# Optimization experiments

Hardware: AMD Instinct MI355X
Metric: run time of the kernel (lower is better)

Reference implementation:

```python
import jax, jax.numpy as jnp
import numpy as np

B, L, E = 4, 1024, 1024
H = 16
HD = E // H
CLIP = 16
SCALE = 1.0 / np.sqrt(HD)


def setup_inputs() -> dict:
    key = jax.random.key(0)
    ks = jax.random.split(key, 13)
    def lin(k, fan_in, fan_out, gain):
        # xavier_uniform
        limit = gain * np.sqrt(6.0 / (fan_in + fan_out))
        return jax.random.uniform(k, (fan_out, fan_in), jnp.float32, -limit, limit)
    inv_sqrt2 = 1.0 / np.sqrt(2.0)
    return {
        "query": jax.random.normal(ks[0], (B, L, E), jnp.float32),
        "key": jax.random.normal(ks[1], (B, L, E), jnp.float32),
        "value": jax.random.normal(ks[2], (B, L, E), jnp.float32),
        "wq": lin(ks[3], E, E, inv_sqrt2), "bq": jnp.zeros((E,), jnp.float32),
        "wk": lin(ks[4], E, E, inv_sqrt2), "bk": jnp.zeros((E,), jnp.float32),
        "wv": lin(ks[5], E, E, inv_sqrt2), "bv": jnp.zeros((E,), jnp.float32),
        "wo": lin(ks[6], E, E, 1.0), "bo": jnp.zeros((E,), jnp.float32),
        "rel_k": jax.random.normal(ks[7], (2 * CLIP + 1, HD), jnp.float32) * 0.02,
        "rel_v": jax.random.normal(ks[8], (2 * CLIP + 1, HD), jnp.float32) * 0.02,
    }


def _heads(x):  # (B, L, E) -> (B, H, L, HD)
    return x.reshape(B, L, H, HD).transpose(0, 2, 1, 3)


def reference(query, key, value, wq, bq, wk, bk, wv, bv, wo, bo, rel_k, rel_v):
    q = _heads(query @ wq.T + bq)
    k = _heads(key @ wk.T + bk)
    v = _heads(value @ wv.T + bv)

    # relative-position index matrix (L_q, L_k), clipped to [-CLIP, CLIP]
    pos = jnp.arange(L)
    dist = jnp.clip(pos[None, :] - pos[:, None], -CLIP, CLIP) + CLIP
    r_k = rel_k[dist]  # (L, L, HD)
    r_v = rel_v[dist]  # (L, L, HD)

    dot = jnp.einsum('bhid,bhjd->bhij', q, k)
    rel = jnp.einsum('bhid,ijd->bhij', q, r_k)
    scores = (dot + rel) * SCALE
    attn = jax.nn.softmax(scores, axis=-1)

    y = jnp.einsum('bhij,bhjd->bhid', attn, v) + jnp.einsum('bhij,ijd->bhid', attn, r_v)
    y = y.transpose(0, 2, 1, 3).reshape(B, L, E)
    return y @ wo.T + bo
```

## Files before the change

kernel.cpp:

```cpp
#include <hip/hip_runtime.h>

#define BB 4
#define LL 1024
#define EE 1024
#define HH 16
#define HD 64
#define NBUCKET 33
#define SCALE 0.125f
#define SC2 (0.125f * 1.44269504088896f)

typedef unsigned short u16;
using f32x4 = __attribute__((ext_vector_type(4))) float;
using s16x8 = __attribute__((ext_vector_type(8))) short;

__device__ __forceinline__ u16 f2bf(float f) {
  union { float f; unsigned u; } x; x.f = f;
  unsigned r = (x.u + 0x7fffu + ((x.u >> 16) & 1u)) >> 16;
  return (u16)r;
}

__device__ __forceinline__ void gld_lds16(const void* g, void* s) {
  __builtin_amdgcn_global_load_lds((const __attribute__((address_space(1))) void*)g,
                                   (__attribute__((address_space(3))) void*)s, 16, 0, 0);
}

__device__ __forceinline__ float qsum16(float s) {
  s += __shfl_xor(s, 1); s += __shfl_xor(s, 2);
  s += __shfl_xor(s, 4); s += __shfl_xor(s, 8);
  return s;
}

__global__ __launch_bounds__(256) void cvt_all(
    const float* __restrict__ q, const float* __restrict__ k, const float* __restrict__ v,
    const float* __restrict__ wq, const float* __restrict__ wk, const float* __restrict__ wv,
    const float* __restrict__ wo, const float* __restrict__ rk,
    u16* __restrict__ oq, u16* __restrict__ ok, u16* __restrict__ ov,
    u16* __restrict__ owq, u16* __restrict__ owk, u16* __restrict__ owv,
    u16* __restrict__ owo, u16* __restrict__ ork) {
  const int bid = blockIdx.x;
  const int tid = threadIdx.x;
  if (bid < 12288) {
    const int z = bid >> 12;
    const int i = (bid & 4095) * 256 + tid;
    const float* in = z == 0 ? q : (z == 1 ? k : v);
    u16* out = z == 0 ? oq : (z == 1 ? ok : ov);
    float4 f = ((const float4*)in)[i];
    ushort4 o;
    o.x = f2bf(f.x); o.y = f2bf(f.y); o.z = f2bf(f.z); o.w = f2bf(f.w);
    ((ushort4*)out)[i] = o;
  } else if (bid < 16384) {
    const int z = (bid - 12288) >> 10;
    const int i = ((bid - 12288) & 1023) * 256 + tid;
    const float* in = z == 0 ? wq : (z == 1 ? wk : (z == 2 ? wv : wo));
    u16* out = z == 0 ? owq : (z == 1 ? owk : (z == 2 ? owv : owo));
    float4 f = ((const float4*)in)[i];
    ushort4 o;
    o.x = f2bf(f.x); o.y = f2bf(f.y); o.z = f2bf(f.z); o.w = f2bf(f.w);
    ((ushort4*)out)[i] = o;
  } else {
    const int i = (bid - 16384) * 256 + tid;
    ork[i] = (i < 33 * 64) ? f2bf(rk[i]) : (u16)0;
  }
}

template <int MODE>
__device__ __forceinline__ void gemm128_bt(const u16* __restrict__ A,
                                           const u16* __restrict__ Bw,
                                           const float* __restrict__ bias,
                                           u16* __restrict__ obf,
                                           float* __restrict__ ofp,
                                           int M, int N, int K, int m0, int n0) {
  __shared__ u16 a_sm[128 * 64];
  __shared__ u16 b_sm[128 * 64];
  const int tid = threadIdx.x;
  const int wave = tid >> 6, lane = tid & 63;
  const int row16 = lane & 15, quad = lane >> 4;
  const int wr = (wave >> 1) * 64, wc = (wave & 1) * 64;
  const int srow = lane >> 3, scol = (lane & 7) * 8;

  f32x4 acc[4][4] = {};

  for (int k0 = 0; k0 < K; k0 += 64) {
#pragma unroll
    for (int t = 0; t < 4; ++t) {
      const int chunk = wave * 4 + t;
      const int r = chunk * 8 + srow;
      gld_lds16(A + (size_t)(m0 + r) * K + k0 + scol, a_sm + chunk * 512);
      gld_lds16(Bw + (size_t)(n0 + r) * K + k0 + scol, b_sm + chunk * 512);
    }
    __syncthreads();
#pragma unroll
    for (int ks = 0; ks < 2; ++ks) {
      s16x8 af[4], bf[4];
#pragma unroll
      for (int mi = 0; mi < 4; ++mi)
        af[mi] = *(const s16x8*)&a_sm[(wr + mi * 16 + row16) * 64 + ks * 32 + quad * 8];
#pragma unroll
      for (int ni = 0; ni < 4; ++ni)
        bf[ni] = *(const s16x8*)&b_sm[(wc + ni * 16 + row16) * 64 + ks * 32 + quad * 8];
#pragma unroll
      for (int mi = 0; mi < 4; ++mi)
#pragma unroll
        for (int ni = 0; ni < 4; ++ni)
          acc[mi][ni] = __builtin_amdgcn_mfma_f32_16x16x32_bf16(af[mi], bf[ni], acc[mi][ni], 0, 0, 0);
    }
    __syncthreads();
  }

#pragma unroll
  for (int mi = 0; mi < 4; ++mi)
#pragma unroll
    for (int ni = 0; ni < 4; ++ni) {
      const int n = n0 + wc + ni * 16 + row16;
      const float bn = bias[n];
      if (MODE == 2) {
        const int mr0 = m0 + wr + mi * 16 + quad * 4;
        const int b = mr0 >> 10, l = mr0 & 1023;
        const int h = n >> 6, hd = n & 63;
        ushort4 o;
        o.x = f2bf(acc[mi][ni][0] + bn);
        o.y = f2bf(acc[mi][ni][1] + bn);
        o.z = f2bf(acc[mi][ni][2] + bn);
        o.w = f2bf(acc[mi][ni][3] + bn);
        *(ushort4*)&obf[((size_t)((b * HH + h) * HD + hd)) * LL + l] = o;
      } else {
#pragma unroll
        for (int r = 0; r < 4; ++r) {
          const int m = m0 + wr + mi * 16 + quad * 4 + r;
          const float v = acc[mi][ni][r] + bn;
          if (MODE == 0) {
            const int b = m >> 10, l = m & 1023, h = n >> 6, hd = n & 63;
            obf[((size_t)((b * HH + h) * LL + l)) * HD + hd] = f2bf(v);
          } else {
            ofp[(size_t)m * N + n] = v;
          }
        }
      }
    }
}

__global__ __launch_bounds__(256) void proj_gemm(
    const u16* __restrict__ xq, const u16* __restrict__ xk, const u16* __restrict__ xv,
    const u16* __restrict__ wqb, const u16* __restrict__ wkb, const u16* __restrict__ wvb,
    const float* __restrict__ bq, const float* __restrict__ bk, const float* __restrict__ bv,
    u16* __restrict__ oq, u16* __restrict__ ok, u16* __restrict__ ovt) {
  if (blockIdx.z == 0)
    gemm128_bt<0>(xq, wqb, bq, oq, nullptr, BB * LL, EE, EE, blockIdx.y * 128, blockIdx.x * 128);
  else if (blockIdx.z == 1)
    gemm128_bt<0>(xk, wkb, bk, ok, nullptr, BB * LL, EE, EE, blockIdx.y * 128, blockIdx.x * 128);
  else
    gemm128_bt<2>(xv, wvb, bv, ovt, nullptr, BB * LL, EE, EE, blockIdx.y * 128, blockIdx.x * 128);
}

__global__ __launch_bounds__(256) void out_gemm(const u16* __restrict__ Y,
                                                const u16* __restrict__ wob,
                                                const float* __restrict__ bo,
                                                float* __restrict__ out) {
  gemm128_bt<1>(Y, wob, bo, nullptr, out, BB * LL, EE, EE, blockIdx.y * 128, blockIdx.x * 128);
}

__global__ __launch_bounds__(256) void attn_fused(
    const u16* __restrict__ Q, const u16* __restrict__ Kb, const u16* __restrict__ Vt,
    const u16* __restrict__ RKp, const float* __restrict__ RV, u16* __restrict__ Y) {
  __shared__ __align__(16) float qr_sm[4][16 * 36];
  __shared__ __align__(16) float s_sm[4][16 * 36];
  __shared__ __align__(16) unsigned char kv[2][17408];

  const int tid = threadIdx.x;
  const int wave = tid >> 6, lane = tid & 63;
  const int row16 = lane & 15, quad = lane >> 4;
  const int bh = blockIdx.x & 63;
  const int i0 = (blockIdx.x >> 6) * 64;
  const int wq0 = i0 + wave * 16;
  const u16* qp = Q + (size_t)bh * LL * HD;
  const char* kpB = (const char*)(Kb + (size_t)bh * LL * HD);
  const char* vpB = (const char*)(Vt + (size_t)bh * HD * LL);

  float* qr_w = &qr_sm[wave][0];
  float* s_w = &s_sm[wave][0];

  int srcK[2], srcV[2];
#pragma unroll
  for (int t = 0; t < 2; ++t) {
    const int cK = (wave * 2 + t) * 64 + lane;
    const int rw = cK >> 3;
    const int cb = ((cK * 16) & 127) ^ ((rw & 7) << 4);
    srcK[t] = rw * 128 + cb;
    srcV[t] = rw * 2048 + cb;
  }
  const int swz = (row16 & 7) << 4;

#pragma unroll
  for (int t = 0; t < 2; ++t) {
    gld_lds16(kpB + srcK[t], kv[0] + (wave * 2 + t) * 1024);
    gld_lds16(vpB + srcV[t], kv[0] + 9216 + (wave * 2 + t) * 1024);
  }

  for (int t = lane; t < 16 * 36; t += 64) s_w[t] = 0.f;

  s16x8 qf[2];
#pragma unroll
  for (int ks = 0; ks < 2; ++ks)
    qf[ks] = *(const s16x8*)(qp + (size_t)(wq0 + row16) * HD + ks * 32 + quad * 8);

  f32x4 a0, a2;
#pragma unroll
  for (int nt = 0; nt < 3; ++nt) {
    f32x4 a = {};
#pragma unroll
    for (int ks = 0; ks < 2; ++ks) {
      s16x8 bfr = *(const s16x8*)(RKp + (size_t)(nt * 16 + row16) * HD + ks * 32 + quad * 8);
      a = __builtin_amdgcn_mfma_f32_16x16x32_bf16(qf[ks], bfr, a, 0, 0, 0);
    }
    if (nt == 0) a0 = a;
    if (nt == 2) a2 = a;
    const int idx = nt * 16 + row16;
    if (idx < NBUCKET)
#pragma unroll
      for (int r = 0; r < 4; ++r) qr_w[(quad * 4 + r) * 36 + idx] = a[r];
  }
  float blo[4], bhi[4];
#pragma unroll
  for (int r = 0; r < 4; ++r) {
    blo[r] = __shfl(a0[r], lane & 48);
    bhi[r] = __shfl(a2[r], lane & 48);
  }

  f32x4 oacc[4] = {};
  float rsum[4] = {0.f, 0.f, 0.f, 0.f};
  float plos[4] = {0.f, 0.f, 0.f, 0.f};
  float phis[4] = {0.f, 0.f, 0.f, 0.f};
  int dbase[4];
#pragma unroll
  for (int nt = 0; nt < 4; ++nt) dbase[nt] = nt * 16 + row16 - quad * 4 - wq0;

  asm volatile("s_waitcnt vmcnt(0) lgkmcnt(0)" ::: "memory");
  __builtin_amdgcn_s_barrier();
  __builtin_amdgcn_sched_barrier(0);

  for (int jt = 0; jt < 16; ++jt) {
    const int j0 = jt * 64;
    unsigned char* kcur = (unsigned char*)kv[jt & 1];
    unsigned char* knxt = (unsigned char*)kv[(jt & 1) ^ 1];
    u16* p_w = (u16*)(kcur) + wave * 1152;

    if (jt < 15) {
      const size_t j1 = (size_t)(j0 + 64);
#pragma unroll
      for (int t = 0; t < 2; ++t) {
        gld_lds16(kpB + j1 * 128 + srcK[t], knxt + (wave * 2 + t) * 1024);
        gld_lds16(vpB + j1 * 2 + srcV[t], knxt + 9216 + (wave * 2 + t) * 1024);
      }
    }

    f32x4 sacc[4] = {};
#pragma unroll
    for (int ks = 0; ks < 2; ++ks)
#pragma unroll
      for (int nt2 = 0; nt2 < 4; ++nt2) {
        const int L = (nt2 * 16 + row16) * 128 + ks * 64 + quad * 16;
        const s16x8 kfr = *(const s16x8*)(kcur + (L ^ swz));
        sacc[nt2] = __builtin_amdgcn_mfma_f32_16x16x32_bf16(qf[ks], kfr, sacc[nt2], 0, 0, 0);
      }
    asm volatile("s_waitcnt lgkmcnt(0)" ::: "memory");
    __builtin_amdgcn_s_barrier();
    __builtin_amdgcn_sched_barrier(0);

    float p[4][4];
    const bool far_lo = (wq0 >= j0 + 79);
    const bool far_hi = (j0 >= wq0 + 31);
    if (far_lo || far_hi) {
#pragma unroll
      for (int r = 0; r < 4; ++r) {
        const float bias = far_lo ? blo[r] : bhi[r];
        float acc = 0.f;
#pragma unroll
        for (int nt2 = 0; nt2 < 4; ++nt2) {
          const float pv = exp2f((sacc[nt2][r] + bias) * SC2);
          p[nt2][r] = pv;
          acc += pv;
        }
        rsum[r] += acc;
        if (far_lo) plos[r] += acc; else phis[r] += acc;
      }
    } else {
#pragma unroll
      for (int nt2 = 0; nt2 < 4; ++nt2)
#pragma unroll
        for (int r = 0; r < 4; ++r) {
          const int dr = dbase[nt2] + j0 - r;
          int bk = dr < -16 ? -16 : (dr > 16 ? 16 : dr);
          bk += 16;
          const float bias = qr_w[(quad * 4 + r) * 36 + bk];
          const float pv = exp2f((sacc[nt2][r] + bias) * SC2);
          p[nt2][r] = pv;
          rsum[r] += pv;
          if (dr <= -16) plos[r] += pv;
          else if (dr >= 16) phis[r] += pv;
          else atomicAdd(&s_w[(quad * 4 + r) * 36 + bk], pv);
        }
    }

#pragma unroll
    for (int nt2 = 0; nt2 < 4; ++nt2) {
      const int c = nt2 * 16 + row16;
#pragma unroll
      for (int rr = 0; rr < 2; ++rr) {
        unsigned pk;
        asm("v_cvt_pk_bf16_f32 %0, %1, %2" : "=v"(pk)
            : "v"(p[nt2][rr * 2]), "v"(p[nt2][rr * 2 + 1]));
        p_w[(quad * 4 + rr * 2) * 72 + c] = (u16)pk;
        p_w[(quad * 4 + rr * 2 + 1) * 72 + c] = (u16)(pk >> 16);
      }
    }

#pragma unroll
    for (int ks = 0; ks < 2; ++ks) {
      const s16x8 pf = *(const s16x8*)&p_w[row16 * 72 + ks * 32 + quad * 8];
#pragma unroll
      for (int dt = 0; dt < 4; ++dt) {
        const int L = (dt * 16 + row16) * 128 + ks * 64 + quad * 16;
        const s16x8 vfr = *(const s16x8*)(kcur + 9216 + (L ^ swz));
        oacc[dt] = __builtin_amdgcn_mfma_f32_16x16x32_bf16(pf, vfr, oacc[dt], 0, 0, 0);
      }
    }

    asm volatile("s_waitcnt vmcnt(0) lgkmcnt(0)" ::: "memory");
    __builtin_amdgcn_s_barrier();
    __builtin_amdgcn_sched_barrier(0);
  }

  float lacc[4], slo[4], shi[4];
#pragma unroll
  for (int r = 0; r < 4; ++r) {
    lacc[r] = qsum16(rsum[r]);
    slo[r] = qsum16(plos[r]);
    shi[r] = qsum16(phis[r]);
  }

  float* rv_sm = (float*)kv[0];
  for (int t = tid; t < NBUCKET * HD; t += 256) rv_sm[t] = RV[t];
  __syncthreads();

  const int b = bh >> 4, h = bh & 15;
#pragma unroll
  for (int r = 0; r < 4; ++r) {
    const int i_loc = quad * 4 + r;
    float rel[4] = {0.f, 0.f, 0.f, 0.f};
    for (int bk = 0; bk < NBUCKET; ++bk) {
      float sv = s_w[i_loc * 36 + bk];
      if (bk == 0) sv += slo[r];
      if (bk == 32) sv += shi[r];
#pragma unroll
      for (int dt = 0; dt < 4; ++dt) rel[dt] += sv * rv_sm[bk * HD + dt * 16 + row16];
    }
    const float inv = 1.0f / lacc[r];
#pragma unroll
    for (int dt = 0; dt < 4; ++dt) {
      const float y = (oacc[dt][r] + rel[dt]) * inv;
      Y[((size_t)(b * LL + wq0 + i_loc)) * EE + h * HD + dt * 16 + row16] = f2bf(y);
    }
  }
}

extern "C" void kernel_launch(void* const* d_in, const int* in_sizes, int n_in,
                              void* d_out, int out_size, void* d_ws, size_t ws_size,
                              hipStream_t stream) {
  const float* query = (const float*)d_in[0];
  const float* key_  = (const float*)d_in[1];
  const float* value = (const float*)d_in[2];
  const float* wq = (const float*)d_in[3];
  const float* bq = (const float*)d_in[4];
  const float* wk = (const float*)d_in[5];
  const float* bk = (const float*)d_in[6];
  const float* wv = (const float*)d_in[7];
  const float* bv = (const float*)d_in[8];
  const float* wo = (const float*)d_in[9];
  const float* bo = (const float*)d_in[10];
  const float* rel_k = (const float*)d_in[11];
  const float* rel_v = (const float*)d_in[12];

  char* base = (char*)d_ws;
  size_t off = 0;
  auto alloc = [&](size_t bytes) -> void* {
    void* p = base + off;
    off += (bytes + 255) & ~(size_t)255;
    return p;
  };
  const size_t XE = (size_t)BB * LL * EE;
  u16* xq    = (u16*)alloc(XE * 2);
  u16* xk    = (u16*)alloc(XE * 2);
  u16* xv    = (u16*)alloc(XE * 2);
  u16* wqb   = (u16*)alloc((size_t)EE * EE * 2);
  u16* wkb   = (u16*)alloc((size_t)EE * EE * 2);
  u16* wvb   = (u16*)alloc((size_t)EE * EE * 2);
  u16* wob   = (u16*)alloc((size_t)EE * EE * 2);
  u16* q_ws  = (u16*)alloc(XE * 2);
  u16* k_ws  = (u16*)alloc(XE * 2);
  u16* vt_ws = (u16*)alloc(XE * 2);
  u16* relkp = (u16*)alloc(48 * 64 * 2);
  u16* y_ws = xq;

  cvt_all<<<16396, 256, 0, stream>>>(query, key_, value, wq, wk, wv, wo, rel_k,
                                     xq, xk, xv, wqb, wkb, wvb, wob, relkp);

  proj_gemm<<<dim3(EE / 128, BB * LL / 128, 3), 256, 0, stream>>>(
      xq, xk, xv, wqb, wkb, wvb, bq, bk, bv, q_ws, k_ws, vt_ws);

  attn_fused<<<1024, 256, 0, stream>>>(q_ws, k_ws, vt_ws, relkp, rel_v, y_ws);

  out_gemm<<<dim3(EE / 128, BB * LL / 128), 256, 0, stream>>>(y_ws, wob, bo, (float*)d_out);
}
```

Baseline: 278.8 us.

## Transpose attention MFMAs to keep P in registers and drop LDS double buffering

Swaps the MFMA operand order so scores come out transposed (key rows per lane, query columns per lane). P can then be repacked in registers with permlane32 swaps instead of a round trip through LDS. A permuted K row mapping lines the score layout up with the PV operand, and the row-sum reductions become cross-quad shuffles. The K/V tile is now single-buffered, so each iteration waits on its own global loads before computing, which gives up the previous load/compute overlap in exchange for less LDS use and fewer LDS writes.

```diff
diff --git a/kernel.cpp b/kernel.cpp
--- a/kernel.cpp
+++ b/kernel.cpp
@@ -22,12 +22,6 @@
 __device__ __forceinline__ void gld_lds16(const void* g, void* s) {
   __builtin_amdgcn_global_load_lds((const __attribute__((address_space(1))) void*)g,
                                    (__attribute__((address_space(3))) void*)s, 16, 0, 0);
-}
-
-__device__ __forceinline__ float qsum16(float s) {
-  s += __shfl_xor(s, 1); s += __shfl_xor(s, 2);
-  s += __shfl_xor(s, 4); s += __shfl_xor(s, 8);
-  return s;
 }
 
 __global__ __launch_bounds__(256) void cvt_all(
@@ -162,9 +156,9 @@
 __global__ __launch_bounds__(256) void attn_fused(
     const u16* __restrict__ Q, const u16* __restrict__ Kb, const u16* __restrict__ Vt,
     const u16* __restrict__ RKp, const float* __restrict__ RV, u16* __restrict__ Y) {
-  __shared__ __align__(16) float qr_sm[4][16 * 36];
+  __shared__ __align__(16) float qr_sm[4][576];
   __shared__ __align__(16) float s_sm[4][16 * 36];
-  __shared__ __align__(16) unsigned char kv[2][17408];
+  __shared__ __align__(16) unsigned char kv[16384];
 
   const int tid = threadIdx.x;
   const int wave = tid >> 6, lane = tid & 63;
@@ -188,12 +182,16 @@
     srcK[t] = rw * 128 + cb;
     srcV[t] = rw * 2048 + cb;
   }
-  const int swz = (row16 & 7) << 4;
+  const int q2 = row16 >> 2;
+  const int prow = ((((q2 << 1) | (q2 >> 1)) & 3) << 2) + (row16 & 3);
+  const int swzK = (prow & 7) << 4;
+  const int swzV = (row16 & 7) << 4;
+  const int rho4 = (((quad << 1) | (quad >> 1)) & 3) << 2;
 
 #pragma unroll
   for (int t = 0; t < 2; ++t) {
-    gld_lds16(kpB + srcK[t], kv[0] + (wave * 2 + t) * 1024);
-    gld_lds16(vpB + srcV[t], kv[0] + 9216 + (wave * 2 + t) * 1024);
+    gld_lds16(kpB + srcK[t], kv + (wave * 2 + t) * 1024);
+    gld_lds16(vpB + srcV[t], kv + 8192 + (wave * 2 + t) * 1024);
   }
 
   for (int t = lane; t < 16 * 36; t += 64) s_w[t] = 0.f;
@@ -209,157 +207,153 @@
     f32x4 a = {};
 #pragma unroll
     for (int ks = 0; ks < 2; ++ks) {
-      s16x8 bfr = *(const s16x8*)(RKp + (size_t)(nt * 16 + row16) * HD + ks * 32 + quad * 8);
-      a = __builtin_amdgcn_mfma_f32_16x16x32_bf16(qf[ks], bfr, a, 0, 0, 0);
+      s16x8 afr = *(const s16x8*)(RKp + (size_t)(nt * 16 + row16) * HD + ks * 32 + quad * 8);
+      a = __builtin_amdgcn_mfma_f32_16x16x32_bf16(afr, qf[ks], a, 0, 0, 0);
     }
     if (nt == 0) a0 = a;
     if (nt == 2) a2 = a;
-    const int idx = nt * 16 + row16;
-    if (idx < NBUCKET)
-#pragma unroll
-      for (int r = 0; r < 4; ++r) qr_w[(quad * 4 + r) * 36 + idx] = a[r];
-  }
-  float blo[4], bhi[4];
-#pragma unroll
-  for (int r = 0; r < 4; ++r) {
-    blo[r] = __shfl(a0[r], lane & 48);
-    bhi[r] = __shfl(a2[r], lane & 48);
-  }
+#pragma unroll
+    for (int r = 0; r < 4; ++r) {
+      const int bk = nt * 16 + quad * 4 + r;
+      if (bk < NBUCKET) qr_w[bk * 17 + row16] = a[r];
+    }
+  }
+  const float blo = __shfl(a0[0], row16);
+  const float bhi = __shfl(a2[0], row16);
 
   f32x4 oacc[4] = {};
-  float rsum[4] = {0.f, 0.f, 0.f, 0.f};
-  float plos[4] = {0.f, 0.f, 0.f, 0.f};
-  float phis[4] = {0.f, 0.f, 0.f, 0.f};
-  int dbase[4];
-#pragma unroll
-  for (int nt = 0; nt < 4; ++nt) dbase[nt] = nt * 16 + row16 - quad * 4 - wq0;
-
-  asm volatile("s_waitcnt vmcnt(0) lgkmcnt(0)" ::: "memory");
-  __builtin_amdgcn_s_barrier();
-  __builtin_amdgcn_sched_barrier(0);
+  float rsum = 0.f, plos = 0.f, phis = 0.f;
+  int baseg[4];
+#pragma unroll
+  for (int g = 0; g < 4; ++g) baseg[g] = g * 16 + rho4 - wq0 - row16;
 
   for (int jt = 0; jt < 16; ++jt) {
     const int j0 = jt * 64;
-    unsigned char* kcur = (unsigned char*)kv[jt & 1];
-    unsigned char* knxt = (unsigned char*)kv[(jt & 1) ^ 1];
-    u16* p_w = (u16*)(kcur) + wave * 1152;
-
-    if (jt < 15) {
-      const size_t j1 = (size_t)(j0 + 64);
+    if (jt) {
 #pragma unroll
       for (int t = 0; t < 2; ++t) {
-        gld_lds16(kpB + j1 * 128 + srcK[t], knxt + (wave * 2 + t) * 1024);
-        gld_lds16(vpB + j1 * 2 + srcV[t], knxt + 9216 + (wave * 2 + t) * 1024);
+        gld_lds16(kpB + (size_t)j0 * 128 + srcK[t], kv + (wave * 2 + t) * 1024);
+        gld_lds16(vpB + (size_t)j0 * 2 + srcV[t], kv + 8192 + (wave * 2 + t) * 1024);
       }
     }
+    asm volatile("s_waitcnt vmcnt(0)" ::: "memory");
+    __builtin_amdgcn_s_barrier();
+    __builtin_amdgcn_sched_barrier(0);
 
     f32x4 sacc[4] = {};
 #pragma unroll
     for (int ks = 0; ks < 2; ++ks)
 #pragma unroll
-      for (int nt2 = 0; nt2 < 4; ++nt2) {
-        const int L = (nt2 * 16 + row16) * 128 + ks * 64 + quad * 16;
-        const s16x8 kfr = *(const s16x8*)(kcur + (L ^ swz));
-        sacc[nt2] = __builtin_amdgcn_mfma_f32_16x16x32_bf16(qf[ks], kfr, sacc[nt2], 0, 0, 0);
+      for (int g = 0; g < 4; ++g) {
+        const int L = (g * 16 + prow) * 128 + ks * 64 + quad * 16;
+        const s16x8 kfr = *(const s16x8*)(kv + (L ^ swzK));
+        sacc[g] = __builtin_amdgcn_mfma_f32_16x16x32_bf16(kfr, qf[ks], sacc[g], 0, 0, 0);
       }
+
+    unsigned pk[4][2];
+    const bool far_lo = (wq0 >= j0 + 79);
+    const bool far_hi = (j0 >= wq0 + 31);
+    if (far_lo || far_hi) {
+      const float bb = (far_lo ? blo : bhi) * SC2;
+      float tacc = 0.f;
+#pragma unroll
+      for (int g = 0; g < 4; ++g)
+#pragma unroll
+        for (int rr = 0; rr < 2; ++rr) {
+          const float pv0 = __builtin_amdgcn_exp2f(sacc[g][rr * 2] * SC2 + bb);
+          const float pv1 = __builtin_amdgcn_exp2f(sacc[g][rr * 2 + 1] * SC2 + bb);
+          tacc += pv0 + pv1;
+          unsigned c;
+          asm("v_cvt_pk_bf16_f32 %0, %1, %2" : "=v"(c) : "v"(pv0), "v"(pv1));
+          pk[g][rr] = c;
+        }
+      rsum += tacc;
+      if (far_lo) plos += tacc; else phis += tacc;
+    } else {
+#pragma unroll
+      for (int g = 0; g < 4; ++g)
+#pragma unroll
+        for (int rr = 0; rr < 2; ++rr) {
+          float pv2[2];
+#pragma unroll
+          for (int e = 0; e < 2; ++e) {
+            const int r = rr * 2 + e;
+            const int dr = baseg[g] + j0 + r;
+            int bk = dr < -16 ? -16 : (dr > 16 ? 16 : dr);
+            bk += 16;
+            const float bias = qr_w[bk * 17 + row16];
+            const float pv = __builtin_amdgcn_exp2f((sacc[g][r] + bias) * SC2);
+            pv2[e] = pv;
+            rsum += pv;
+            if (dr <= -16) plos += pv;
+            else if (dr >= 16) phis += pv;
+            else atomicAdd(&s_w[row16 * 36 + bk], pv);
+          }
+          unsigned c;
+          asm("v_cvt_pk_bf16_f32 %0, %1, %2" : "=v"(c) : "v"(pv2[0]), "v"(pv2[1]));
+          pk[g][rr] = c;
+        }
+    }
+
+    s16x8 pf[2];
+#pragma unroll
+    for (int ks = 0; ks < 2; ++ks) {
+      unsigned x0 = pk[ks * 2][0], y0 = pk[ks * 2 + 1][0];
+      unsigned x1 = pk[ks * 2][1], y1 = pk[ks * 2 + 1][1];
+      asm("v_permlane32_swap_b32 %0, %1" : "+v"(x0), "+v"(y0));
+      asm("v_permlane32_swap_b32 %0, %1" : "+v"(x1), "+v"(y1));
+      union { unsigned u[4]; s16x8 v; } pfu;
+      pfu.u[0] = x0; pfu.u[1] = x1; pfu.u[2] = y0; pfu.u[3] = y1;
+      pf[ks] = pfu.v;
+    }
+
+#pragma unroll
+    for (int ks = 0; ks < 2; ++ks)
+#pragma unroll
+      for (int dt = 0; dt < 4; ++dt) {
+        const int L = (dt * 16 + row16) * 128 + ks * 64 + quad * 16;
+        const s16x8 vfr = *(const s16x8*)(kv + 8192 + (L ^ swzV));
+        oacc[dt] = __builtin_amdgcn_mfma_f32_16x16x32_bf16(vfr, pf[ks], oacc[dt], 0, 0, 0);
+      }
+
     asm volatile("s_waitcnt lgkmcnt(0)" ::: "memory");
     __builtin_amdgcn_s_barrier();
     __builtin_amdgcn_sched_barrier(0);
-
-    float p[4][4];
-    const bool far_lo = (wq0 >= j0 + 79);
-    const bool far_hi = (j0 >= wq0 + 31);
-    if (far_lo || far_hi) {
-#pragma unroll
-      for (int r = 0; r < 4; ++r) {
-        const float bias = far_lo ? blo[r] : bhi[r];
-        float acc = 0.f;
-#pragma unroll
-        for (int nt2 = 0; nt2 < 4; ++nt2) {
-          const float pv = exp2f((sacc[nt2][r] + bias) * SC2);
-          p[nt2][r] = pv;
-          acc += pv;
-        }
-        rsum[r] += acc;
-        if (far_lo) plos[r] += acc; else phis[r] += acc;
-      }
-    } else {
-#pragma unroll
-      for (int nt2 = 0; nt2 < 4; ++nt2)
-#pragma unroll
-        for (int r = 0; r < 4; ++r) {
-          const int dr = dbase[nt2] + j0 - r;
-          int bk = dr < -16 ? -16 : (dr > 16 ? 16 : dr);
-          bk += 16;
-          const float bias = qr_w[(quad * 4 + r) * 36 + bk];
-          const float pv = exp2f((sacc[nt2][r] + bias) * SC2);
-          p[nt2][r] = pv;
-          rsum[r] += pv;
-          if (dr <= -16) plos[r] += pv;
-          else if (dr >= 16) phis[r] += pv;
-          else atomicAdd(&s_w[(quad * 4 + r) * 36 + bk], pv);
-        }
-    }
-
-#pragma unroll
-    for (int nt2 = 0; nt2 < 4; ++nt2) {
-      const int c = nt2 * 16 + row16;
-#pragma unroll
-      for (int rr = 0; rr < 2; ++rr) {
-        unsigned pk;
-        asm("v_cvt_pk_bf16_f32 %0, %1, %2" : "=v"(pk)
-            : "v"(p[nt2][rr * 2]), "v"(p[nt2][rr * 2 + 1]));
-        p_w[(quad * 4 + rr * 2) * 72 + c] = (u16)pk;
-        p_w[(quad * 4 + rr * 2 + 1) * 72 + c] = (u16)(pk >> 16);
-      }
-    }
-
-#pragma unroll
-    for (int ks = 0; ks < 2; ++ks) {
-      const s16x8 pf = *(const s16x8*)&p_w[row16 * 72 + ks * 32 + quad * 8];
-#pragma unroll
-      for (int dt = 0; dt < 4; ++dt) {
-        const int L = (dt * 16 + row16) * 128 + ks * 64 + quad * 16;
-        const s16x8 vfr = *(const s16x8*)(kcur + 9216 + (L ^ swz));
-        oacc[dt] = __builtin_amdgcn_mfma_f32_16x16x32_bf16(pf, vfr, oacc[dt], 0, 0, 0);
-      }
-    }
-
-    asm volatile("s_waitcnt vmcnt(0) lgkmcnt(0)" ::: "memory");
-    __builtin_amdgcn_s_barrier();
-    __builtin_amdgcn_sched_barrier(0);
-  }
-
-  float lacc[4], slo[4], shi[4];
-#pragma unroll
-  for (int r = 0; r < 4; ++r) {
-    lacc[r] = qsum16(rsum[r]);
-    slo[r] = qsum16(plos[r]);
-    shi[r] = qsum16(phis[r]);
-  }
-
-  float* rv_sm = (float*)kv[0];
+  }
+
+  float t1 = rsum + __shfl_xor(rsum, 16);
+  const float lacc = t1 + __shfl_xor(t1, 32);
+  t1 = plos + __shfl_xor(plos, 16);
+  const float slo = t1 + __shfl_xor(t1, 32);
+  t1 = phis + __shfl_xor(phis, 16);
+  const float shi = t1 + __shfl_xor(t1, 32);
+
+  float* rv_sm = (float*)kv;
   for (int t = tid; t < NBUCKET * HD; t += 256) rv_sm[t] = RV[t];
   __syncthreads();
 
   const int b = bh >> 4, h = bh & 15;
-#pragma unroll
-  for (int r = 0; r < 4; ++r) {
-    const int i_loc = quad * 4 + r;
-    float rel[4] = {0.f, 0.f, 0.f, 0.f};
-    for (int bk = 0; bk < NBUCKET; ++bk) {
-      float sv = s_w[i_loc * 36 + bk];
-      if (bk == 0) sv += slo[r];
-      if (bk == 32) sv += shi[r];
-#pragma unroll
-      for (int dt = 0; dt < 4; ++dt) rel[dt] += sv * rv_sm[bk * HD + dt * 16 + row16];
-    }
-    const float inv = 1.0f / lacc[r];
+  float rel[4][4] = {};
+  for (int bk = 0; bk < NBUCKET; ++bk) {
+    float sv = s_w[row16 * 36 + bk];
+    if (bk == 0) sv += slo;
+    if (bk == 32) sv += shi;
 #pragma unroll
     for (int dt = 0; dt < 4; ++dt) {
-      const float y = (oacc[dt][r] + rel[dt]) * inv;
-      Y[((size_t)(b * LL + wq0 + i_loc)) * EE + h * HD + dt * 16 + row16] = f2bf(y);
-    }
+      const f32x4 rv4 = *(const f32x4*)&rv_sm[bk * HD + dt * 16 + quad * 4];
+#pragma unroll
+      for (int r = 0; r < 4; ++r) rel[dt][r] += sv * rv4[r];
+    }
+  }
+  const float inv = 1.0f / lacc;
+#pragma unroll
+  for (int dt = 0; dt < 4; ++dt) {
+    ushort4 o;
+    o.x = f2bf((oacc[dt][0] + rel[dt][0]) * inv);
+    o.y = f2bf((oacc[dt][1] + rel[dt][1]) * inv);
+    o.z = f2bf((oacc[dt][2] + rel[dt][2]) * inv);
+    o.w = f2bf((oacc[dt][3] + rel[dt][3]) * inv);
+    *(ushort4*)&Y[((size_t)(b * LL + wq0 + row16)) * EE + h * HD + dt * 16 + quad * 4] = o;
   }
 }
 
```

After: 250.7 us. -10.1%, faster.
